# Optimization experiments

Measured on AMD Instinct MI355X. Metric: run time of the kernel, lower is better.

Reference implementation:

```python
import jax, jax.numpy as jnp
import numpy as np

B, S, D = 4, 4096, 2048
H, HD = 16, 128
TILE = 16
N_TILES = 8


def setup_inputs() -> dict:
    key = jax.random.key(0)
    ks = jax.random.split(key, 6)
    x = jax.random.normal(ks[0], (B, S, D), dtype=jnp.float32)
    anchor_indices = jax.random.randint(ks[1], (B, H, N_TILES), 0, S // TILE).astype(jnp.int32)
    sc = 1.0 / np.sqrt(D)
    Wq = jax.random.normal(ks[2], (D, H * HD), dtype=jnp.float32) * sc
    Wk = jax.random.normal(ks[3], (D, H * HD), dtype=jnp.float32) * sc
    Wv = jax.random.normal(ks[4], (D, H * HD), dtype=jnp.float32) * sc
    Wo = jax.random.normal(ks[5], (H * HD, D), dtype=jnp.float32) * (1.0 / np.sqrt(H * HD))
    return {"x": x, "anchor_indices": anchor_indices, "Wq": Wq, "Wk": Wk, "Wv": Wv, "Wo": Wo}


def reference(x, anchor_indices, Wq, Wk, Wv, Wo):
    batch, seq_len, _ = x.shape
    # QKV projections -> (b, h, s, d)
    q = (x @ Wq).reshape(batch, seq_len, H, HD).transpose(0, 2, 1, 3)
    k = (x @ Wk).reshape(batch, seq_len, H, HD).transpose(0, 2, 1, 3)
    v = (x @ Wv).reshape(batch, seq_len, H, HD).transpose(0, 2, 1, 3)
    # Force last tile slot to the current local tile (causal local attention)
    current_tile_idx = (seq_len - 1) // TILE
    tiles = anchor_indices.at[:, :, -1].set(current_tile_idx)
    # Expand tile indices to token indices: (b, h, n_tiles*TILE)
    token_indices = (tiles[..., None] * TILE + jnp.arange(TILE)[None, None, None, :]).reshape(batch, H, -1)
    # Gather sparse K/V per head: (b, h, K, d)
    k_sparse = jnp.take_along_axis(k, token_indices[..., None], axis=2)
    v_sparse = jnp.take_along_axis(v, token_indices[..., None], axis=2)
    logits = jnp.einsum('bhqd,bhkd->bhqk', q, k_sparse) / jnp.sqrt(jnp.float32(HD))
    # Causal mask over gathered (non-contiguous) key positions
    future_mask = token_indices[:, :, None, :] > jnp.arange(seq_len)[None, None, :, None]
    logits = jnp.where(future_mask, -1e10, logits)
    weights = jax.nn.softmax(logits, axis=-1)
    out = jnp.einsum('bhqk,bhkd->bhqd', weights, v_sparse)
    out = out.transpose(0, 2, 1, 3).reshape(batch, seq_len, H * HD)
    return out @ Wo
```

## Files before the change

### kernel.cpp

```cpp
#include <hip/hip_runtime.h>
#include <stdint.h>

#define Bz 4
#define Sz 4096
#define Dz 2048
#define Hz 16
#define HDz 128
#define NTz 8
#define TILEz 16

typedef __bf16 bf16x8 __attribute__((ext_vector_type(8)));
typedef float f32x4 __attribute__((ext_vector_type(4)));
typedef float fx4 __attribute__((ext_vector_type(4)));
typedef unsigned short u16;
typedef u16 u16x4 __attribute__((ext_vector_type(4)));
typedef u16 u16x8 __attribute__((ext_vector_type(8)));

#define MFMA16(a, b, c) __builtin_amdgcn_mfma_f32_16x16x32_bf16((a), (b), (c), 0, 0, 0)

__device__ __forceinline__ u16 f2bf(float f) {
    uint32_t u = __builtin_bit_cast(uint32_t, f);
    return (u16)((u + 0x7fffu + ((u >> 16) & 1u)) >> 16);
}

__device__ __forceinline__ void async16(const u16* g, u16* l) {
    __builtin_amdgcn_global_load_lds(
        (const __attribute__((address_space(1))) unsigned int*)(g),
        (__attribute__((address_space(3))) unsigned int*)(l), 16, 0, 0);
}

__global__ void cvt_x(const float* __restrict__ x, u16* __restrict__ o) {
    int i = blockIdx.x * 256 + threadIdx.x;
    const fx4* xv = (const fx4*)x;
    fx4 a = xv[i * 2], b = xv[i * 2 + 1];
    u16x8 r;
    r[0] = f2bf(a[0]); r[1] = f2bf(a[1]); r[2] = f2bf(a[2]); r[3] = f2bf(a[3]);
    r[4] = f2bf(b[0]); r[5] = f2bf(b[1]); r[6] = f2bf(b[2]); r[7] = f2bf(b[3]);
    ((u16x8*)o)[i] = r;
}

__global__ void transpose_cvt(const float* W0, const float* W1, const float* W2, const float* W3,
                              u16* O0, u16* O1, u16* O2, u16* O3) {
    const float* W; u16* O;
    switch (blockIdx.z) {
        case 0: W = W0; O = O0; break;
        case 1: W = W1; O = O1; break;
        case 2: W = W2; O = O2; break;
        default: W = W3; O = O3; break;
    }
    __shared__ u16 tile[32][33];
    int bx = blockIdx.x * 32, by = blockIdx.y * 32;
    int tx = threadIdx.x, ty = threadIdx.y;
#pragma unroll
    for (int i = 0; i < 32; i += 8)
        tile[ty + i][tx] = f2bf(W[(long)(by + ty + i) * 2048 + bx + tx]);
    __syncthreads();
#pragma unroll
    for (int i = 0; i < 32; i += 8)
        O[(long)(bx + ty + i) * 2048 + by + tx] = tile[tx][ty + i];
}

template <typename OutT>
__global__ __launch_bounds__(256) void gemm_bt(const u16* __restrict__ A, const u16* __restrict__ BT,
                                               OutT* __restrict__ C, int M_, int N_, int K_) {
    __shared__ __align__(16) u16 As[4096];
    __shared__ __align__(16) u16 Bs[4096];
    const int t = threadIdx.x, w = t >> 6, l = t & 63, lr = l & 15, quad = l >> 4;
    const int bn = blockIdx.x, bm = blockIdx.y;
    const u16* gA[2]; const u16* gB[2]; u16* lA[2]; u16* lB[2];
#pragma unroll
    for (int r = 0; r < 2; r++) {
        int c = r * 256 + t;
        gA[r] = A + (long)(bm * 128 + (c >> 2)) * K_ + (c & 3) * 8;
        gB[r] = BT + (long)(bn * 128 + (c >> 2)) * K_ + (c & 3) * 8;
        lA[r] = &As[(r * 256 + w * 64) * 8];
        lB[r] = &Bs[(r * 256 + w * 64) * 8];
    }
    f32x4 acc[4][4] = {};
    const int wr = (w >> 1) * 64, wc = (w & 1) * 64;
    for (int k0 = 0; k0 < K_; k0 += 32) {
        async16(gA[0] + k0, lA[0]); async16(gA[1] + k0, lA[1]);
        async16(gB[0] + k0, lB[0]); async16(gB[1] + k0, lB[1]);
        __syncthreads();
        bf16x8 af[4], bfr[4];
#pragma unroll
        for (int i = 0; i < 4; i++) af[i] = *(const bf16x8*)&As[(wr + i * 16 + lr) * 32 + quad * 8];
#pragma unroll
        for (int j = 0; j < 4; j++) bfr[j] = *(const bf16x8*)&Bs[(wc + j * 16 + lr) * 32 + quad * 8];
#pragma unroll
        for (int i = 0; i < 4; i++)
#pragma unroll
            for (int j = 0; j < 4; j++) acc[i][j] = MFMA16(af[i], bfr[j], acc[i][j]);
        __syncthreads();
    }
#pragma unroll
    for (int i = 0; i < 4; i++) {
        int row0 = bm * 128 + wr + i * 16 + quad * 4;
#pragma unroll
        for (int j = 0; j < 4; j++) {
            int col = bn * 128 + wc + j * 16 + lr;
#pragma unroll
            for (int rg = 0; rg < 4; rg++) {
                long idx = (long)(row0 + rg) * N_ + col;
                if constexpr (sizeof(OutT) == 2) ((u16*)C)[idx] = f2bf(acc[i][j][rg]);
                else ((float*)C)[idx] = acc[i][j][rg];
            }
        }
    }
}

#define KV_SPLIT 4
#define KV_CHUNK (Dz / KV_SPLIT)
__global__ __launch_bounds__(256) void kv_sparse(const u16* __restrict__ xbf, const u16* __restrict__ WkT,
                                                 const u16* __restrict__ WvT, const int* __restrict__ anchor,
                                                 float* __restrict__ part) {
    const int bh = blockIdx.x, which = blockIdx.y, split = blockIdx.z;
    const int b = bh >> 4, h = bh & 15;
    __shared__ int toks[128];
    __shared__ __align__(16) u16 As[4096];
    __shared__ __align__(16) u16 Bs[4096];
    const int t = threadIdx.x, w = t >> 6, l = t & 63, lr = l & 15, quad = l >> 4;
    if (t < 128) {
        int j = t >> 4;
        int tile = (j == 7) ? (Sz / TILEz - 1) : anchor[bh * NTz + j];
        toks[t] = tile * TILEz + (t & 15);
    }
    __syncthreads();
    const u16* gA[2]; const u16* gB[2]; u16* lA[2]; u16* lB[2];
#pragma unroll
    for (int r = 0; r < 2; r++) {
        int c = r * 256 + t;
        int row = c >> 2, col8 = (c & 3) * 8;
        const u16* xrow = xbf + ((long)b * Sz + toks[row]) * Dz + col8;
        const u16* wrowK = WkT + (long)(h * HDz + row) * Dz + col8;
        const u16* wrowV = WvT + (long)(h * HDz + row) * Dz + col8;
        gA[r] = (which == 0) ? xrow : wrowV;
        gB[r] = (which == 0) ? wrowK : xrow;
        lA[r] = &As[(r * 256 + w * 64) * 8];
        lB[r] = &Bs[(r * 256 + w * 64) * 8];
    }
    f32x4 acc[4][4] = {};
    const int wr = (w >> 1) * 64, wc = (w & 1) * 64;
    const int ks0 = split * KV_CHUNK;
    for (int k0 = ks0; k0 < ks0 + KV_CHUNK; k0 += 32) {
        async16(gA[0] + k0, lA[0]); async16(gA[1] + k0, lA[1]);
        async16(gB[0] + k0, lB[0]); async16(gB[1] + k0, lB[1]);
        __syncthreads();
        bf16x8 af[4], bfr[4];
#pragma unroll
        for (int i = 0; i < 4; i++) af[i] = *(const bf16x8*)&As[(wr + i * 16 + lr) * 32 + quad * 8];
#pragma unroll
        for (int j = 0; j < 4; j++) bfr[j] = *(const bf16x8*)&Bs[(wc + j * 16 + lr) * 32 + quad * 8];
#pragma unroll
        for (int i = 0; i < 4; i++)
#pragma unroll
            for (int j = 0; j < 4; j++) acc[i][j] = MFMA16(af[i], bfr[j], acc[i][j]);
        __syncthreads();
    }
    float* out = part + (((long)split * 2 + which) * 64 + bh) * 16384;
#pragma unroll
    for (int i = 0; i < 4; i++) {
        int row0 = wr + i * 16 + quad * 4;
#pragma unroll
        for (int j = 0; j < 4; j++) {
            int col = wc + j * 16 + lr;
#pragma unroll
            for (int rg = 0; rg < 4; rg++) out[(row0 + rg) * 128 + col] = acc[i][j][rg];
        }
    }
}

__global__ void kv_reduce(const float* __restrict__ part, u16* __restrict__ kv) {
    long i = ((long)blockIdx.x * 256 + threadIdx.x) * 4;
    const long stride = 2L * 64 * 16384;
    fx4 s = *(const fx4*)(part + i);
#pragma unroll
    for (int sp = 1; sp < KV_SPLIT; sp++) {
        fx4 p = *(const fx4*)(part + sp * stride + i);
        s[0] += p[0]; s[1] += p[1]; s[2] += p[2]; s[3] += p[3];
    }
    u16x4 r;
    r[0] = f2bf(s[0]); r[1] = f2bf(s[1]); r[2] = f2bf(s[2]); r[3] = f2bf(s[3]);
    *(u16x4*)(kv + i) = r;
}

__global__ __launch_bounds__(256) void attn_kernel(u16* QAO,
                                                   const u16* __restrict__ ksp, const u16* __restrict__ vspT,
                                                   const int* __restrict__ anchor) {
    const int st = blockIdx.x, h = blockIdx.y, b = blockIdx.z;
    const int bh = b * Hz + h, s0 = st * 128;
    __shared__ __align__(16) u16 Ps[128 * 136];
    __shared__ int toks[128];
    const int t = threadIdx.x, w = t >> 6, l = t & 63, lr = l & 15, quad = l >> 4;
    if (t < 128) {
        int j = t >> 4;
        int tile = (j == 7) ? (Sz / TILEz - 1) : anchor[bh * NTz + j];
        toks[t] = tile * TILEz + (t & 15);
    }
    __syncthreads();
    const u16* Qb = QAO + (long)(b * Sz + s0 + w * 32) * 2048 + h * HDz;
    const u16* Kb = ksp + (long)bh * HDz * 128;
    const u16* Vb = vspT + (long)bh * HDz * 128;
    f32x4 acc[2][8] = {};
#pragma unroll
    for (int ks = 0; ks < 4; ks++) {
        bf16x8 a0 = *(const bf16x8*)(Qb + (long)lr * 2048 + ks * 32 + quad * 8);
        bf16x8 a1 = *(const bf16x8*)(Qb + (long)(16 + lr) * 2048 + ks * 32 + quad * 8);
#pragma unroll
        for (int j = 0; j < 8; j++) {
            bf16x8 bj = *(const bf16x8*)(Kb + (j * 16 + lr) * 128 + ks * 32 + quad * 8);
            acc[0][j] = MFMA16(a0, bj, acc[0][j]);
            acc[1][j] = MFMA16(a1, bj, acc[1][j]);
        }
    }
    int tokj[8];
#pragma unroll
    for (int j = 0; j < 8; j++) tokj[j] = toks[j * 16 + lr];
    const float scale = 0.08838834764831845f;
#pragma unroll
    for (int i = 0; i < 2; i++) {
#pragma unroll
        for (int rg = 0; rg < 4; rg++) {
            int qpos = s0 + w * 32 + i * 16 + quad * 4 + rg;
            float v[8];
#pragma unroll
            for (int j = 0; j < 8; j++)
                v[j] = (tokj[j] > qpos) ? -1e10f : acc[i][j][rg] * scale;
            float mx = v[0];
#pragma unroll
            for (int j = 1; j < 8; j++) mx = fmaxf(mx, v[j]);
            mx = fmaxf(mx, __shfl_xor(mx, 1, 64));
            mx = fmaxf(mx, __shfl_xor(mx, 2, 64));
            mx = fmaxf(mx, __shfl_xor(mx, 4, 64));
            mx = fmaxf(mx, __shfl_xor(mx, 8, 64));
            float s = 0.f;
#pragma unroll
            for (int j = 0; j < 8; j++) { v[j] = exp2f((v[j] - mx) * 1.4426950408889634f); s += v[j]; }
            s += __shfl_xor(s, 1, 64);
            s += __shfl_xor(s, 2, 64);
            s += __shfl_xor(s, 4, 64);
            s += __shfl_xor(s, 8, 64);
            float rs = 1.0f / s;
            int prow = w * 32 + i * 16 + quad * 4 + rg;
#pragma unroll
            for (int j = 0; j < 8; j++) Ps[prow * 136 + j * 16 + lr] = f2bf(v[j] * rs);
        }
    }
    __syncthreads();
    f32x4 oacc[2][8] = {};
#pragma unroll
    for (int ks = 0; ks < 4; ks++) {
        bf16x8 a0 = *(const bf16x8*)(Vb + (w * 32 + lr) * 128 + ks * 32 + quad * 8);
        bf16x8 a1 = *(const bf16x8*)(Vb + (w * 32 + 16 + lr) * 128 + ks * 32 + quad * 8);
#pragma unroll
        for (int j = 0; j < 8; j++) {
            bf16x8 bj = *(const bf16x8*)&Ps[(j * 16 + lr) * 136 + ks * 32 + quad * 8];
            oacc[0][j] = MFMA16(a0, bj, oacc[0][j]);
            oacc[1][j] = MFMA16(a1, bj, oacc[1][j]);
        }
    }
#pragma unroll
    for (int i = 0; i < 2; i++) {
#pragma unroll
        for (int j = 0; j < 8; j++) {
            u16x4 pk;
#pragma unroll
            for (int rg = 0; rg < 4; rg++) pk[rg] = f2bf(oacc[i][j][rg]);
            int d = w * 32 + i * 16 + quad * 4;
            int q = j * 16 + lr;
            *(u16x4*)(QAO + (long)(b * Sz + s0 + q) * 2048 + h * HDz + d) = pk;
        }
    }
}

extern "C" void kernel_launch(void* const* d_in, const int* in_sizes, int n_in,
                              void* d_out, int out_size, void* d_ws, size_t ws_size,
                              hipStream_t stream) {
    const float* x = (const float*)d_in[0];
    const int* anchor = (const int*)d_in[1];
    const float* Wq = (const float*)d_in[2];
    const float* Wk = (const float*)d_in[3];
    const float* Wv = (const float*)d_in[4];
    const float* Wo = (const float*)d_in[5];

    char* ws = (char*)d_ws;
    const size_t XB = 67108864;
    const size_t WB = 8388608;
    u16* xbf = (u16*)(ws);
    u16* WqT = (u16*)(ws + XB);
    u16* WkT = (u16*)(ws + XB + WB);
    u16* WvT = (u16*)(ws + XB + 2 * WB);
    u16* WoT = (u16*)(ws + XB + 3 * WB);
    u16* Qb  = (u16*)(ws + XB + 4 * WB);
    float* kvpart = (float*)(ws + XB + 4 * WB);
    u16* ksp = (u16*)(ws + 2 * XB + 4 * WB);
    u16* vspT= (u16*)(ws + 2 * XB + 4 * WB + 2097152);

    cvt_x<<<16384, 256, 0, stream>>>(x, xbf);
    transpose_cvt<<<dim3(64, 64, 4), dim3(32, 8), 0, stream>>>(Wq, Wk, Wv, Wo, WqT, WkT, WvT, WoT);
    kv_sparse<<<dim3(64, 2, KV_SPLIT), 256, 0, stream>>>(xbf, WkT, WvT, anchor, kvpart);
    kv_reduce<<<2048, 256, 0, stream>>>(kvpart, ksp);
    gemm_bt<u16><<<dim3(16, 128), 256, 0, stream>>>(xbf, WqT, Qb, 16384, 2048, 2048);
    attn_kernel<<<dim3(32, 16, 4), 256, 0, stream>>>(Qb, ksp, vspT, anchor);
    gemm_bt<float><<<dim3(16, 128), 256, 0, stream>>>(Qb, WoT, (float*)d_out, 16384, 2048, 2048);
}
```

Baseline: 748.4 us.

## Replace 128x128 GEMM with 256x256 pipelined, swizzled 512-thread GEMM

Replaces the simple 128x128-tile GEMM used for the Q projection and output projection with a 256x256-tile kernel that runs 8 waves. It triple-buffers its LDS stages using async global-to-LDS loads with explicit vmcnt waits, and adds an XOR swizzle on LDS columns to avoid bank conflicts. It also remaps block IDs for L2 locality and raises wave priority around the MFMA bursts. The aim is more data reuse per loaded tile and hiding memory latency behind compute; the cost is 128KB of LDS per block, which limits occupancy, and more delicate barrier and waitcnt correctness.

```diff
diff --git a/kernel.cpp b/kernel.cpp
--- a/kernel.cpp
+++ b/kernel.cpp
@@ -28,6 +28,13 @@
         (const __attribute__((address_space(1))) unsigned int*)(g),
         (__attribute__((address_space(3))) unsigned int*)(l), 16, 0, 0);
 }
+
+#define BAR()                                  \
+    do {                                       \
+        asm volatile("" ::: "memory");         \
+        __builtin_amdgcn_s_barrier();          \
+        asm volatile("" ::: "memory");         \
+    } while (0)
 
 __global__ void cvt_x(const float* __restrict__ x, u16* __restrict__ o) {
     int i = blockIdx.x * 256 + threadIdx.x;
@@ -60,50 +67,101 @@
         O[(long)(bx + ty + i) * 2048 + by + tx] = tile[tx][ty + i];
 }
 
+__device__ __forceinline__ void stage2(const u16* s0, const u16* s1, u16* chunk, int w, int koff) {
+    async16(s0 + koff, chunk + w * 512);
+    async16(s1 + koff, chunk + w * 512 + 4096);
+}
+
 template <typename OutT>
-__global__ __launch_bounds__(256) void gemm_bt(const u16* __restrict__ A, const u16* __restrict__ BT,
-                                               OutT* __restrict__ C, int M_, int N_, int K_) {
-    __shared__ __align__(16) u16 As[4096];
-    __shared__ __align__(16) u16 Bs[4096];
+__global__ __launch_bounds__(512, 2) void gemm256(const u16* __restrict__ A, const u16* __restrict__ BT,
+                                                  OutT* __restrict__ C, int M_, int N_, int K_) {
+    __shared__ __align__(1024) u16 lds[65536];
     const int t = threadIdx.x, w = t >> 6, l = t & 63, lr = l & 15, quad = l >> 4;
-    const int bn = blockIdx.x, bm = blockIdx.y;
-    const u16* gA[2]; const u16* gB[2]; u16* lA[2]; u16* lB[2];
+    const int wm = w >> 2, wn = w & 3;
+    const int nbn = N_ >> 8;
+    const int cpx = gridDim.x >> 3;
+    const int swz = (blockIdx.x & 7) * cpx + (blockIdx.x >> 3);
+    const int bm = swz / nbn, bn = swz % nbn;
+
+    const u16* sA[2]; const u16* sB[2];
 #pragma unroll
     for (int r = 0; r < 2; r++) {
-        int c = r * 256 + t;
-        gA[r] = A + (long)(bm * 128 + (c >> 2)) * K_ + (c & 3) * 8;
-        gB[r] = BT + (long)(bn * 128 + (c >> 2)) * K_ + (c & 3) * 8;
-        lA[r] = &As[(r * 256 + w * 64) * 8];
-        lB[r] = &Bs[(r * 256 + w * 64) * 8];
-    }
-    f32x4 acc[4][4] = {};
-    const int wr = (w >> 1) * 64, wc = (w & 1) * 64;
-    for (int k0 = 0; k0 < K_; k0 += 32) {
-        async16(gA[0] + k0, lA[0]); async16(gA[1] + k0, lA[1]);
-        async16(gB[0] + k0, lB[0]); async16(gB[1] + k0, lB[1]);
-        __syncthreads();
-        bf16x8 af[4], bfr[4];
-#pragma unroll
-        for (int i = 0; i < 4; i++) af[i] = *(const bf16x8*)&As[(wr + i * 16 + lr) * 32 + quad * 8];
-#pragma unroll
-        for (int j = 0; j < 4; j++) bfr[j] = *(const bf16x8*)&Bs[(wc + j * 16 + lr) * 32 + quad * 8];
-#pragma unroll
-        for (int i = 0; i < 4; i++)
-#pragma unroll
-            for (int j = 0; j < 4; j++) acc[i][j] = MFMA16(af[i], bfr[j], acc[i][j]);
-        __syncthreads();
-    }
-#pragma unroll
-    for (int i = 0; i < 4; i++) {
-        int row0 = bm * 128 + wr + i * 16 + quad * 4;
-#pragma unroll
-        for (int j = 0; j < 4; j++) {
-            int col = bn * 128 + wc + j * 16 + lr;
-#pragma unroll
-            for (int rg = 0; rg < 4; rg++) {
-                long idx = (long)(row0 + rg) * N_ + col;
-                if constexpr (sizeof(OutT) == 2) ((u16*)C)[idx] = f2bf(acc[i][j][rg]);
-                else ((float*)C)[idx] = acc[i][j][rg];
+        int idx = r * 512 + t;
+        int row = idx >> 2;
+        int q = (t & 3) ^ ((row >> 2) & 2);
+        sA[r] = A + (long)(bm * 256 + row) * K_ + q * 8;
+        sB[r] = BT + (long)(bn * 256 + row) * K_ + q * 8;
+    }
+    const int qro = (quad ^ (((lr >> 3) & 1) << 1)) * 8;
+    const int rowA0 = wm * 128 + lr;
+    const int rowB0 = wn * 64 + lr;
+    const int nt = K_ >> 6;
+
+    f32x4 acc[8][4] = {};
+
+    stage2(sA[0], sA[1], lds + 0, w, 0);
+    stage2(sB[0], sB[1], lds + 32768, w, 0);
+    stage2(sA[0], sA[1], lds + 8192, w, 32);
+    stage2(sB[0], sB[1], lds + 32768 + 8192, w, 32);
+    const int k1 = (nt > 1) ? 64 : 0;
+    stage2(sA[0], sA[1], lds + 16384, w, k1);
+    stage2(sB[0], sB[1], lds + 32768 + 16384, w, k1);
+    asm volatile("s_waitcnt vmcnt(4)" ::: "memory");
+    BAR();
+
+    for (int g = 0; g < nt; ++g) {
+        const int cb = g & 1, ob = cb ^ 1;
+        const int t1k = ((g + 1 < nt ? g + 1 : nt - 1) << 6) + 32;
+        const int t2k = ((g + 2 < nt ? g + 2 : nt - 1) << 6);
+        const u16* Abase = lds + cb * 16384;
+        const u16* Bbase = lds + 32768 + cb * 16384;
+#pragma unroll
+        for (int kh = 0; kh < 2; ++kh) {
+            const u16* Ach = Abase + kh * 8192;
+            const u16* Bch = Bbase + kh * 8192;
+            bf16x8 bfr[4];
+#pragma unroll
+            for (int j = 0; j < 4; ++j)
+                bfr[j] = *(const bf16x8*)(Bch + (rowB0 + j * 16) * 32 + qro);
+#pragma unroll
+            for (int mh = 0; mh < 2; ++mh) {
+                bf16x8 af[4];
+#pragma unroll
+                for (int i = 0; i < 4; ++i)
+                    af[i] = *(const bf16x8*)(Ach + (rowA0 + mh * 64 + i * 16) * 32 + qro);
+                if (kh == 0 && mh == 0)      stage2(sA[0], sA[1], lds + ob * 16384 + 8192, w, t1k);
+                else if (kh == 0 && mh == 1) stage2(sB[0], sB[1], lds + 32768 + ob * 16384 + 8192, w, t1k);
+                else if (kh == 1 && mh == 0) stage2(sA[0], sA[1], lds + cb * 16384, w, t2k);
+                else                         stage2(sB[0], sB[1], lds + 32768 + cb * 16384, w, t2k);
+                asm volatile("" ::: "memory");
+                __builtin_amdgcn_s_barrier();
+                asm volatile("s_waitcnt lgkmcnt(0)" ::: "memory");
+                __builtin_amdgcn_s_setprio(1);
+#pragma unroll
+                for (int i = 0; i < 4; ++i)
+#pragma unroll
+                    for (int j = 0; j < 4; ++j)
+                        acc[mh * 4 + i][j] = MFMA16(af[i], bfr[j], acc[mh * 4 + i][j]);
+                __builtin_amdgcn_s_setprio(0);
+                if (kh == 1 && mh == 1) asm volatile("s_waitcnt vmcnt(4)" ::: "memory");
+                BAR();
+            }
+        }
+    }
+
+    const long crow0 = (long)bm * 256 + wm * 128;
+    const int ccol0 = bn * 256 + wn * 64;
+#pragma unroll
+    for (int f = 0; f < 8; ++f) {
+        long row0 = crow0 + (f >> 2) * 64 + (f & 3) * 16 + quad * 4;
+#pragma unroll
+        for (int j = 0; j < 4; ++j) {
+            int col = ccol0 + j * 16 + lr;
+#pragma unroll
+            for (int rg = 0; rg < 4; ++rg) {
+                long idx = (row0 + rg) * N_ + col;
+                if constexpr (sizeof(OutT) == 2) ((u16*)C)[idx] = f2bf(acc[f][j][rg]);
+                else ((float*)C)[idx] = acc[f][j][rg];
             }
         }
     }
@@ -300,7 +358,7 @@
     transpose_cvt<<<dim3(64, 64, 4), dim3(32, 8), 0, stream>>>(Wq, Wk, Wv, Wo, WqT, WkT, WvT, WoT);
     kv_sparse<<<dim3(64, 2, KV_SPLIT), 256, 0, stream>>>(xbf, WkT, WvT, anchor, kvpart);
     kv_reduce<<<2048, 256, 0, stream>>>(kvpart, ksp);
-    gemm_bt<u16><<<dim3(16, 128), 256, 0, stream>>>(xbf, WqT, Qb, 16384, 2048, 2048);
+    gemm256<u16><<<dim3(512), dim3(512), 0, stream>>>(xbf, WqT, Qb, 16384, 2048, 2048);
     attn_kernel<<<dim3(32, 16, 4), 256, 0, stream>>>(Qb, ksp, vspT, anchor);
-    gemm_bt<float><<<dim3(16, 128), 256, 0, stream>>>(Qb, WoT, (float*)d_out, 16384, 2048, 2048);
-}
+    gemm256<float><<<dim3(512), dim3(512), 0, stream>>>(Qb, WoT, (float*)d_out, 16384, 2048, 2048);
+}
```

Result: faster. 628.8 us (-16.0%).
